# Kernel tuning notes

Hardware: AMD Instinct MI355X
Metric: run time of the kernel (lower is better)

## Reference

```python
import jax, jax.numpy as jnp
import numpy as np
from jax import lax

EPS = 1e-8
NUM_CLASSES = 10
OUT_DIM = 16
IN_CAPS = 32 * 6 * 6  # 1152
IN_DIM = 8
NUM_ITERS = 3


def squash(x, axis=-1):
    norm = jnp.sum(x * x, axis=axis, keepdims=True)
    return norm / (norm + 1.0) * x / (jnp.sqrt(norm) + EPS)


def conv2d(x, w, b, stride):
    y = lax.conv_general_dilated(x, w, window_strides=(stride, stride), padding='VALID',
                                 dimension_numbers=('NCHW', 'OIHW', 'NCHW'))
    return y + b[None, :, None, None]


def setup_inputs() -> dict:
    key = jax.random.key(0)
    ks = jax.random.split(key, 12)
    B = 256
    inp = {}
    inp['x'] = jax.random.normal(ks[0], (B, 1, 28, 28), dtype=jnp.float32)
    inp['y'] = jax.random.randint(ks[1], (B,), 0, NUM_CLASSES)
    s = 0.05
    inp['conv1_w'] = jax.random.normal(ks[2], (256, 1, 9, 9), dtype=jnp.float32) * s
    inp['conv1_b'] = jnp.zeros((256,), dtype=jnp.float32)
    inp['prim_w'] = jax.random.normal(ks[3], (32 * 8, 256, 9, 9), dtype=jnp.float32) * s
    inp['prim_b'] = jnp.zeros((32 * 8,), dtype=jnp.float32)
    # torch init is randn; scaled down mildly for numerical sanity
    inp['route_W'] = jax.random.normal(ks[4], (NUM_CLASSES, IN_CAPS, IN_DIM, OUT_DIM), dtype=jnp.float32) * 0.1
    inp['dec_w1'] = jax.random.normal(ks[5], (NUM_CLASSES * OUT_DIM, 512), dtype=jnp.float32) * s
    inp['dec_b1'] = jnp.zeros((512,), dtype=jnp.float32)
    inp['dec_w2'] = jax.random.normal(ks[6], (512, 1024), dtype=jnp.float32) * s
    inp['dec_b2'] = jnp.zeros((1024,), dtype=jnp.float32)
    inp['dec_w3'] = jax.random.normal(ks[7], (1024, 28 * 28), dtype=jnp.float32) * s
    inp['dec_b3'] = jnp.zeros((28 * 28,), dtype=jnp.float32)
    return inp


def reference(x, y, conv1_w, conv1_b, prim_w, prim_b, route_W,
              dec_w1, dec_b1, dec_w2, dec_b2, dec_w3, dec_b3):
    B = x.shape[0]
    # conv1 + relu: [B,256,20,20]
    h = jax.nn.relu(conv2d(x, conv1_w, conv1_b, stride=1))
    # primary capsules: conv stride 2 -> [B,256,6,6] -> [B,1152,8], squash
    p = conv2d(h, prim_w, prim_b, stride=2)
    u = squash(p.reshape(B, -1, IN_DIM))  # [B,1152,8]
    # routing: u_hat [B,C,N,D]
    u_hat = jnp.einsum('bnd,cnde->bcne', u, route_W)
    b_logits = jnp.zeros_like(u_hat)
    for _ in range(NUM_ITERS - 1):
        c = jax.nn.softmax(b_logits, axis=2)
        s = jnp.sum(c * u_hat, axis=2, keepdims=True)  # [B,C,1,D]
        v = squash(s)
        b_logits = b_logits + u_hat * v
    c = jax.nn.softmax(b_logits, axis=2)
    s = jnp.sum(c * u_hat, axis=2, keepdims=True)
    v = squash(s)[:, :, 0, :]  # [B,C,D]
    logits = jax.nn.softmax(jnp.sqrt(jnp.sum(v * v, axis=-1)), axis=-1)  # [B,C]
    y_onehot = jax.nn.one_hot(y, NUM_CLASSES, dtype=v.dtype)  # [B,C]
    d = (v * y_onehot[:, :, None]).reshape(B, -1)  # [B,160]
    d = jax.nn.relu(d @ dec_w1 + dec_b1)
    d = jax.nn.relu(d @ dec_w2 + dec_b2)
    recons = d @ dec_w3 + dec_b3  # [B,784]
    return logits, recons
```

## Files before the change

### kernel.cpp

```cpp
#include <hip/hip_runtime.h>
#include <hip/hip_fp16.h>
#include <math.h>

#define EPS 1e-8f
#define AS1 __attribute__((address_space(1)))
#define AS3 __attribute__((address_space(3)))

typedef _Float16 f16x8 __attribute__((ext_vector_type(8)));
typedef float f32x4 __attribute__((ext_vector_type(4)));

__global__ __launch_bounds__(256) void transpose_k(const float* __restrict__ in,
                                                   float* __restrict__ out, int R, int C) {
    __shared__ float tile[64][65];
    int tx = threadIdx.x & 63, ty = threadIdx.x >> 6;
    int c0 = blockIdx.x * 64, r0 = blockIdx.y * 64;
#pragma unroll
    for (int i = 0; i < 16; ++i) {
        int r = r0 + ty + i * 4, c = c0 + tx;
        if (r < R && c < C) tile[ty + i * 4][tx] = in[(long)r * C + c];
    }
    __syncthreads();
#pragma unroll
    for (int i = 0; i < 16; ++i) {
        int r = c0 + ty + i * 4, c = r0 + tx;
        if (r < C && c < R) out[(long)r * R + c] = tile[tx][ty + i * 4];
    }
}

__global__ __launch_bounds__(256) void wprep_k(const float* __restrict__ prim_w,
                                               __half* __restrict__ w2) {
    __shared__ float pl[128 * 81];
    int t = threadIdx.x, co = blockIdx.x, cih = blockIdx.y;
    for (int i = t; i < 10368; i += 256) pl[i] = prim_w[co * 20736 + cih * 10368 + i];
    __syncthreads();
    for (int o = t; o < 10368; o += 256) {
        int tap = o >> 7, cil = o & 127;
        w2[(long)co * 20736 + tap * 256 + cih * 128 + cil] = __float2half(pl[cil * 81 + tap]);
    }
}

__global__ __launch_bounds__(256) void conv1_k(const float* __restrict__ x,
                                               const float* __restrict__ wt1,
                                               const float* __restrict__ bias,
                                               __half* __restrict__ hh) {
    __shared__ float img[784];
    __shared__ float wl2[81 * 128];
    int t = threadIdx.x, b = blockIdx.x;
    int chalf = blockIdx.y >> 1, ph = blockIdx.y & 1;
    for (int i = t; i < 784; i += 256) img[i] = x[b * 784 + i];
    for (int i = t; i < 81 * 128; i += 256) {
        int tap = i >> 7, j = i & 127;
        wl2[i] = wt1[tap * 256 + chalf * 128 + j];
    }
    __syncthreads();
    int lane = t & 63, grp = t >> 6;
    int col = lane * 2;
    float2 cb = *(const float2*)&bias[chalf * 128 + col];
    int ow0 = ph * 10;
    for (int oh = grp * 5; oh < grp * 5 + 5; ++oh) {
        float acc0[10], acc1[10];
#pragma unroll
        for (int p = 0; p < 10; ++p) { acc0[p] = 0.f; acc1[p] = 0.f; }
#pragma unroll
        for (int kh = 0; kh < 9; ++kh) {
            float r[19];
            const float* irow = &img[(oh + kh) * 28 + ow0];
#pragma unroll
            for (int q = 0; q < 19; ++q) r[q] = irow[q];
#pragma unroll
            for (int kw = 0; kw < 9; ++kw) {
                float2 wv = *(const float2*)&wl2[(kh * 9 + kw) * 128 + col];
#pragma unroll
                for (int p = 0; p < 10; ++p) {
                    acc0[p] += r[kw + p] * wv.x;
                    acc1[p] += r[kw + p] * wv.y;
                }
            }
        }
#pragma unroll
        for (int p = 0; p < 10; ++p) {
            int pix = oh * 20 + ow0 + p;
            __half2 hv;
            hv.x = __float2half(fmaxf(acc0[p] + cb.x, 0.f));
            hv.y = __float2half(fmaxf(acc1[p] + cb.y, 0.f));
            *(__half2*)&hh[((long)b * 400 + pix) * 256 + chalf * 128 + col] = hv;
        }
    }
}

__global__ __launch_bounds__(256) void primgemm_k(const __half* __restrict__ hh,
                                                  const __half* __restrict__ w2,
                                                  float* __restrict__ Cpart) {
    __shared__ __align__(16) char lds[2][32768];
    const int t = threadIdx.x;
    const int lane = t & 63, w = t >> 6;
    const int l15 = lane & 15, kl = lane >> 4;
    const int sw = l15 & 7;

    const int bx = blockIdx.x;
    const int mt = bx >> 3, nb = (bx >> 2) & 1, ks = bx & 3;
    const int mr = w >> 1, nc = w & 1;

    long wsrc[4], asrc[4];
    int dstW[4];
#pragma unroll
    for (int q = 0; q < 4; ++q) {
        int row = q * 32 + w * 8 + (lane >> 3);
        int lc = (lane & 7) ^ (row & 7);
        dstW[q] = q * 4096 + w * 1024;
        wsrc[q] = (long)(nb * 128 + row) * 20736 + ks * 64 + lc * 8;
        int m = mt * 128 + row;
        int bi = m / 36, pos = m - bi * 36;
        int oy = pos / 6, ox = pos - oy * 6;
        asrc[q] = ((long)bi * 400 + oy * 40 + ox * 2) * 256 + ks * 64 + lc * 8;
    }

    f32x4 acc[4][4];
#pragma unroll
    for (int i = 0; i < 4; ++i)
#pragma unroll
        for (int j = 0; j < 4; ++j) acc[i][j] = (f32x4){0.f, 0.f, 0.f, 0.f};

    auto stage = [&](int bufi, int tap) {
        int kh = tap / 9, kw = tap - kh * 9;
        int woff = tap * 256;
        int aoff = (kh * 20 + kw) * 256;
#pragma unroll
        for (int q = 0; q < 4; ++q)
            __builtin_amdgcn_global_load_lds((const AS1 void*)(w2 + wsrc[q] + woff),
                                             (AS3 void*)(&lds[bufi][dstW[q]]), 16, 0, 0);
#pragma unroll
        for (int q = 0; q < 4; ++q)
            __builtin_amdgcn_global_load_lds((const AS1 void*)(hh + asrc[q] + aoff),
                                             (AS3 void*)(&lds[bufi][16384 + dstW[q]]), 16, 0, 0);
    };

    int wrowb[4], arowb[4], rdoff[2];
#pragma unroll
    for (int f = 0; f < 4; ++f) {
        wrowb[f] = (nc * 64 + f * 16 + l15) * 128;
        arowb[f] = 16384 + (mr * 64 + f * 16 + l15) * 128;
    }
#pragma unroll
    for (int kc = 0; kc < 2; ++kc) rdoff[kc] = ((kc * 4 + kl) ^ sw) << 4;

    stage(0, 0);
    __syncthreads();
    int buf = 0;
    for (int s = 0; s < 81; ++s) {
        if (s < 80) stage(buf ^ 1, s + 1);
        const char* B = lds[buf];
#pragma unroll
        for (int kc = 0; kc < 2; ++kc) {
            f16x8 wf[4], af[4];
#pragma unroll
            for (int nf = 0; nf < 4; ++nf) wf[nf] = *(const f16x8*)(B + wrowb[nf] + rdoff[kc]);
#pragma unroll
            for (int mf = 0; mf < 4; ++mf) af[mf] = *(const f16x8*)(B + arowb[mf] + rdoff[kc]);
#pragma unroll
            for (int mf = 0; mf < 4; ++mf)
#pragma unroll
                for (int nf = 0; nf < 4; ++nf)
                    acc[mf][nf] = __builtin_amdgcn_mfma_f32_16x16x32_f16(wf[nf], af[mf],
                                                                         acc[mf][nf], 0, 0, 0);
        }
        __syncthreads();
        buf ^= 1;
    }

    float* Cp = Cpart + (long)ks * 2359296;
#pragma unroll
    for (int mf = 0; mf < 4; ++mf)
#pragma unroll
        for (int nf = 0; nf < 4; ++nf) {
            int m = mt * 128 + mr * 64 + mf * 16 + l15;
            int co = nb * 128 + nc * 64 + nf * 16 + kl * 4;
            *(f32x4*)(Cp + (long)m * 256 + co) = acc[mf][nf];
        }
}

__global__ __launch_bounds__(256) void squashp_k(const float* __restrict__ Cpart,
                                                 const float* __restrict__ bias,
                                                 float* __restrict__ u) {
    __shared__ float sm[9216];
    __shared__ float bs[256];
    int t = threadIdx.x, b = blockIdx.x;
    bs[t] = bias[t];
    for (int i = t; i < 9216; i += 256) {
        float s = 0.f;
#pragma unroll
        for (int ks = 0; ks < 4; ++ks) s += Cpart[(long)ks * 2359296 + (long)b * 9216 + i];
        sm[i] = s;
    }
    __syncthreads();
    for (int cap = t; cap < 1152; cap += 256) {
        float xs[8], sn = 0.f;
#pragma unroll
        for (int d = 0; d < 8; ++d) {
            int f = cap * 8 + d;
            int co = f / 36, pos = f - co * 36;
            float vv = sm[pos * 256 + co] + bs[co];
            xs[d] = vv;
            sn += vv * vv;
        }
        float sc = sn / ((sn + 1.f) * (sqrtf(sn) + EPS));
#pragma unroll
        for (int d = 0; d < 8; ++d) u[(long)b * 9216 + cap * 8 + d] = xs[d] * sc;
    }
}

__global__ __launch_bounds__(256) void uhat_k(const float* __restrict__ u,
                                              const float* __restrict__ W,
                                              __half* __restrict__ uh) {
    __shared__ float wl[32 * 132];
    int t = threadIdx.x;
    int c = blockIdx.x / 36, ng = blockIdx.x - c * 36;
    const float* Wc = W + (long)c * 147456 + ng * 4096;
    for (int i = t; i < 4096; i += 256) {
        int row = i >> 7, k = i & 127;
        wl[row * 132 + k] = Wc[i];
    }
    __syncthreads();
    int nl = t >> 3, bl = t & 7;
    int n = ng * 32 + nl;
    const float* wr = &wl[nl * 132];
    for (int bq = 0; bq < 32; ++bq) {
        int b = bq * 8 + bl;
        const float* ub = u + (long)b * 9216 + n * 8;
        float4 ua = *(const float4*)ub, uv = *(const float4*)(ub + 4);
        float ud[8] = {ua.x, ua.y, ua.z, ua.w, uv.x, uv.y, uv.z, uv.w};
        float acc[16];
#pragma unroll
        for (int e = 0; e < 16; ++e) acc[e] = 0.f;
#pragma unroll
        for (int d = 0; d < 8; ++d) {
            const float* wd = wr + d * 16;
#pragma unroll
            for (int eq = 0; eq < 4; ++eq) {
                float4 wq = *(const float4*)(wd + eq * 4);
                acc[eq * 4 + 0] += ud[d] * wq.x;
                acc[eq * 4 + 1] += ud[d] * wq.y;
                acc[eq * 4 + 2] += ud[d] * wq.z;
                acc[eq * 4 + 3] += ud[d] * wq.w;
            }
        }
        f16x8 o0, o1;
#pragma unroll
        for (int e = 0; e < 8; ++e) {
            o0[e] = (_Float16)acc[e];
            o1[e] = (_Float16)acc[8 + e];
        }
        __half* dst = uh + ((long)(c * 256 + b)) * 18432 + n * 16;
        *(f16x8*)dst = o0;
        *(f16x8*)(dst + 8) = o1;
    }
}

__global__ __launch_bounds__(256) void route2_k(const __half* __restrict__ uh,
                                                float* __restrict__ v) {
    __shared__ float red[4][18];
    int t = threadIdx.x;
    int c = blockIdx.x >> 8, b = blockIdx.x & 255;
    int lane = t & 63, w = t >> 6;
    const float valid4 = (t < 128) ? 1.f : 0.f;
    const __half* ub = uh + ((long)(c * 256 + b)) * 18432;

    f16x8 uhh[5][2];
#pragma unroll
    for (int i = 0; i < 5; ++i) {
        int n = (i == 4) ? ((t < 128) ? 1024 + t : 0) : (t + 256 * i);
        const __half* p = ub + n * 16;
        uhh[i][0] = *(const f16x8*)p;
        uhh[i][1] = *(const f16x8*)(p + 8);
    }

    float vsum[16], sv[16];
#pragma unroll
    for (int e = 0; e < 16; ++e) vsum[e] = 0.f;

    for (int iter = 0; iter < 3; ++iter) {
        float li[5];
        float pmax = -1e30f;
#pragma unroll
        for (int i = 0; i < 5; ++i) {
            float s = 0.f;
#pragma unroll
            for (int e = 0; e < 16; ++e) s += (float)uhh[i][e >> 3][e & 7] * vsum[e];
            li[i] = s;
            float sm = (i == 4 && valid4 == 0.f) ? -1e30f : s;
            pmax = fmaxf(pmax, sm);
        }
#pragma unroll
        for (int m = 1; m < 64; m <<= 1) pmax = fmaxf(pmax, __shfl_xor(pmax, m, 64));
        if (lane == 0) red[w][17] = pmax;
        __syncthreads();
        float M = fmaxf(fmaxf(red[0][17], red[1][17]), fmaxf(red[2][17], red[3][17]));

        float pe = 0.f, se[16];
#pragma unroll
        for (int e = 0; e < 16; ++e) se[e] = 0.f;
#pragma unroll
        for (int i = 0; i < 5; ++i) {
            float E = __expf(li[i] - M);
            if (i == 4) E *= valid4;
            pe += E;
#pragma unroll
            for (int e = 0; e < 16; ++e) se[e] += E * (float)uhh[i][e >> 3][e & 7];
        }
#pragma unroll
        for (int m = 1; m < 64; m <<= 1) {
            pe += __shfl_xor(pe, m, 64);
#pragma unroll
            for (int e = 0; e < 16; ++e) se[e] += __shfl_xor(se[e], m, 64);
        }
        if (lane == 0) {
            red[w][16] = pe;
#pragma unroll
            for (int e = 0; e < 16; ++e) red[w][e] = se[e];
        }
        __syncthreads();
        float peT = red[0][16] + red[1][16] + red[2][16] + red[3][16];
        float rp = 1.f / peT;
        float nrm = 0.f;
#pragma unroll
        for (int e = 0; e < 16; ++e) {
            sv[e] = (red[0][e] + red[1][e] + red[2][e] + red[3][e]) * rp;
            nrm += sv[e] * sv[e];
        }
        float sc = nrm / ((nrm + 1.f) * (sqrtf(nrm) + EPS));
#pragma unroll
        for (int e = 0; e < 16; ++e) {
            sv[e] *= sc;
            vsum[e] += sv[e];
        }
        __syncthreads();
    }
    if (t == 0) {
#pragma unroll
        for (int e = 0; e < 16; ++e) v[(b * 10 + c) * 16 + e] = sv[e];
    }
}

__global__ __launch_bounds__(256) void logits_k(const float* __restrict__ v,
                                                float* __restrict__ out) {
    int b = threadIdx.x;
    float nr[10];
#pragma unroll
    for (int c = 0; c < 10; ++c) {
        float s2 = 0.f;
#pragma unroll
        for (int e = 0; e < 16; ++e) {
            float xv = v[(b * 10 + c) * 16 + e];
            s2 += xv * xv;
        }
        nr[c] = sqrtf(s2);
    }
    float mx = nr[0];
#pragma unroll
    for (int c = 1; c < 10; ++c) mx = fmaxf(mx, nr[c]);
    float ex[10], sm = 0.f;
#pragma unroll
    for (int c = 0; c < 10; ++c) {
        ex[c] = __expf(nr[c] - mx);
        sm += ex[c];
    }
#pragma unroll
    for (int c = 0; c < 10; ++c) out[b * 10 + c] = ex[c] / sm;
}

__global__ __launch_bounds__(256) void fc1_k(const float* __restrict__ v,
                                             const int* __restrict__ y,
                                             const float* __restrict__ w1,
                                             const float* __restrict__ b1,
                                             float* __restrict__ h1) {
    int b = blockIdx.x, t = threadIdx.x;
    __shared__ float vs[16];
    int cls = y[b];
    if (t < 16) vs[t] = v[(b * 10 + cls) * 16 + t];
    __syncthreads();
    for (int j = t; j < 512; j += 256) {
        float a = b1[j];
#pragma unroll
        for (int d = 0; d < 16; ++d) a += vs[d] * w1[(cls * 16 + d) * 512 + j];
        h1[b * 512 + j] = fmaxf(a, 0.f);
    }
}

__global__ __launch_bounds__(256) void fc_k(const float* __restrict__ A,
                                            const float* __restrict__ Wt,
                                            const float* __restrict__ bias,
                                            float* __restrict__ C,
                                            int K, int N, int relu) {
    __shared__ float al[8 * 1024];
    int t = threadIdx.x;
    int j = blockIdx.x * 256 + t;
    int r0 = blockIdx.y * 8;
    for (int idx = t; idx < 8 * K; idx += 256) {
        int r = idx / K, kk = idx - r * K;
        al[r * K + kk] = A[(r0 + r) * K + kk];
    }
    __syncthreads();
    if (j < N) {
        float bj = bias[j];
        float acc[8];
#pragma unroll
        for (int i = 0; i < 8; ++i) acc[i] = bj;
        for (int k = 0; k < K; ++k) {
            float w = Wt[(long)k * N + j];
#pragma unroll
            for (int i = 0; i < 8; ++i) acc[i] += al[i * K + k] * w;
        }
#pragma unroll
        for (int i = 0; i < 8; ++i) {
            float o = acc[i];
            if (relu) o = fmaxf(o, 0.f);
            C[(r0 + i) * N + j] = o;
        }
    }
}

extern "C" void kernel_launch(void* const* d_in, const int* in_sizes, int n_in,
                              void* d_out, int out_size, void* d_ws, size_t ws_size,
                              hipStream_t stream) {
    (void)in_sizes; (void)n_in; (void)out_size; (void)ws_size;
    const float* x       = (const float*)d_in[0];
    const int*   y       = (const int*)d_in[1];
    const float* conv1_w = (const float*)d_in[2];
    const float* conv1_b = (const float*)d_in[3];
    const float* prim_w  = (const float*)d_in[4];
    const float* prim_b  = (const float*)d_in[5];
    const float* route_W = (const float*)d_in[6];
    const float* dec_w1  = (const float*)d_in[7];
    const float* dec_b1  = (const float*)d_in[8];
    const float* dec_w2  = (const float*)d_in[9];
    const float* dec_b2  = (const float*)d_in[10];
    const float* dec_w3  = (const float*)d_in[11];
    const float* dec_b3  = (const float*)d_in[12];
    float* out = (float*)d_out;

    float* ws  = (float*)d_ws;
    float* Cp  = ws;
    float* u   = Cp + 9437184;
    float* wt1 = u + 2359296;
    float* v   = wt1 + 20736;
    float* h1  = v + 40960;
    float* h2  = h1 + 131072;
    __half* hh = (__half*)(h2 + 262144);
    __half* w2 = hh + 26214400;
    __half* uhb = hh;

    hipLaunchKernelGGL(transpose_k, dim3(2, 4), dim3(256), 0, stream, conv1_w, wt1, 256, 81);
    hipLaunchKernelGGL(wprep_k, dim3(256, 2), dim3(256), 0, stream, prim_w, w2);
    hipLaunchKernelGGL(conv1_k, dim3(256, 4), dim3(256), 0, stream, x, wt1, conv1_b, hh);
    hipLaunchKernelGGL(primgemm_k, dim3(576), dim3(256), 0, stream, hh, w2, Cp);
    hipLaunchKernelGGL(squashp_k, dim3(256), dim3(256), 0, stream, Cp, prim_b, u);
    hipLaunchKernelGGL(uhat_k, dim3(360), dim3(256), 0, stream, u, route_W, uhb);
    hipLaunchKernelGGL(route2_k, dim3(2560), dim3(256), 0, stream, uhb, v);
    hipLaunchKernelGGL(logits_k, dim3(1), dim3(256), 0, stream, v, out);
    hipLaunchKernelGGL(fc1_k, dim3(256), dim3(256), 0, stream, v, y, dec_w1, dec_b1, h1);
    hipLaunchKernelGGL(fc_k, dim3(4, 32), dim3(256), 0, stream, h1, dec_w2, dec_b2, h2, 512, 1024, 1);
    hipLaunchKernelGGL(fc_k, dim3(4, 32), dim3(256), 0, stream, h2, dec_w3, dec_b3, out + 2560, 1024, 784, 0);
}
```

Baseline: 581.3 us.

## Load primary-capsule A operand directly into registers instead of via LDS

In the primary-capsule implicit GEMM, the activation (A) tiles are now read from global memory straight into per-lane MFMA fragment registers, double-buffered across taps, rather than staged through LDS with global_load_lds. Only the weight tile stays in LDS, which halves LDS use and removes LDS reads for A. The trade-off is more register pressure, and each wave now issues its own A loads instead of sharing a staged tile, so the same data may be fetched redundantly by the wave pairs that share rows.

```diff
diff --git a/kernel.cpp b/kernel.cpp
--- a/kernel.cpp
+++ b/kernel.cpp
@@ -91,7 +91,7 @@
 __global__ __launch_bounds__(256) void primgemm_k(const __half* __restrict__ hh,
                                                   const __half* __restrict__ w2,
                                                   float* __restrict__ Cpart) {
-    __shared__ __align__(16) char lds[2][32768];
+    __shared__ __align__(16) char lds[2][16384];
     const int t = threadIdx.x;
     const int lane = t & 63, w = t >> 6;
     const int l15 = lane & 15, kl = lane >> 4;
@@ -101,7 +101,7 @@
     const int mt = bx >> 3, nb = (bx >> 2) & 1, ks = bx & 3;
     const int mr = w >> 1, nc = w & 1;
 
-    long wsrc[4], asrc[4];
+    long wsrc[4];
     int dstW[4];
 #pragma unroll
     for (int q = 0; q < 4; ++q) {
@@ -109,10 +109,15 @@
         int lc = (lane & 7) ^ (row & 7);
         dstW[q] = q * 4096 + w * 1024;
         wsrc[q] = (long)(nb * 128 + row) * 20736 + ks * 64 + lc * 8;
-        int m = mt * 128 + row;
+    }
+
+    long abase[4];
+#pragma unroll
+    for (int mf = 0; mf < 4; ++mf) {
+        int m = mt * 128 + mr * 64 + mf * 16 + l15;
         int bi = m / 36, pos = m - bi * 36;
         int oy = pos / 6, ox = pos - oy * 6;
-        asrc[q] = ((long)bi * 400 + oy * 40 + ox * 2) * 256 + ks * 64 + lc * 8;
+        abase[mf] = ((long)bi * 400 + oy * 40 + ox * 2) * 256 + ks * 64 + kl * 8;
     }
 
     f32x4 acc[4][4];
@@ -122,51 +127,62 @@
         for (int j = 0; j < 4; ++j) acc[i][j] = (f32x4){0.f, 0.f, 0.f, 0.f};
 
     auto stage = [&](int bufi, int tap) {
-        int kh = tap / 9, kw = tap - kh * 9;
         int woff = tap * 256;
-        int aoff = (kh * 20 + kw) * 256;
 #pragma unroll
         for (int q = 0; q < 4; ++q)
             __builtin_amdgcn_global_load_lds((const AS1 void*)(w2 + wsrc[q] + woff),
                                              (AS3 void*)(&lds[bufi][dstW[q]]), 16, 0, 0);
-#pragma unroll
-        for (int q = 0; q < 4; ++q)
-            __builtin_amdgcn_global_load_lds((const AS1 void*)(hh + asrc[q] + aoff),
-                                             (AS3 void*)(&lds[bufi][16384 + dstW[q]]), 16, 0, 0);
     };
-
-    int wrowb[4], arowb[4], rdoff[2];
-#pragma unroll
-    for (int f = 0; f < 4; ++f) {
-        wrowb[f] = (nc * 64 + f * 16 + l15) * 128;
-        arowb[f] = 16384 + (mr * 64 + f * 16 + l15) * 128;
-    }
+    auto loadA = [&](f16x8 (&dst)[4][2], int tap) {
+        int kh = tap / 9, kw = tap - kh * 9;
+        int aoff = (kh * 20 + kw) * 256;
+#pragma unroll
+        for (int mf = 0; mf < 4; ++mf)
+#pragma unroll
+            for (int kc = 0; kc < 2; ++kc)
+                dst[mf][kc] = *(const f16x8*)(hh + abase[mf] + aoff + kc * 32);
+    };
+
+    int wrowb[4], rdoff[2];
+#pragma unroll
+    for (int f = 0; f < 4; ++f) wrowb[f] = (nc * 64 + f * 16 + l15) * 128;
 #pragma unroll
     for (int kc = 0; kc < 2; ++kc) rdoff[kc] = ((kc * 4 + kl) ^ sw) << 4;
 
+    auto compute = [&](const char* B, f16x8 (&ar)[4][2]) {
+#pragma unroll
+        for (int kc = 0; kc < 2; ++kc) {
+            f16x8 wf[4];
+#pragma unroll
+            for (int nf = 0; nf < 4; ++nf) wf[nf] = *(const f16x8*)(B + wrowb[nf] + rdoff[kc]);
+#pragma unroll
+            for (int mf = 0; mf < 4; ++mf)
+#pragma unroll
+                for (int nf = 0; nf < 4; ++nf)
+                    acc[mf][nf] = __builtin_amdgcn_mfma_f32_16x16x32_f16(wf[nf], ar[mf][kc],
+                                                                         acc[mf][nf], 0, 0, 0);
+        }
+    };
+
+    f16x8 aA[4][2], aB[4][2];
+    loadA(aA, 0);
     stage(0, 0);
     __syncthreads();
     int buf = 0;
-    for (int s = 0; s < 81; ++s) {
-        if (s < 80) stage(buf ^ 1, s + 1);
-        const char* B = lds[buf];
-#pragma unroll
-        for (int kc = 0; kc < 2; ++kc) {
-            f16x8 wf[4], af[4];
-#pragma unroll
-            for (int nf = 0; nf < 4; ++nf) wf[nf] = *(const f16x8*)(B + wrowb[nf] + rdoff[kc]);
-#pragma unroll
-            for (int mf = 0; mf < 4; ++mf) af[mf] = *(const f16x8*)(B + arowb[mf] + rdoff[kc]);
-#pragma unroll
-            for (int mf = 0; mf < 4; ++mf)
-#pragma unroll
-                for (int nf = 0; nf < 4; ++nf)
-                    acc[mf][nf] = __builtin_amdgcn_mfma_f32_16x16x32_f16(wf[nf], af[mf],
-                                                                         acc[mf][nf], 0, 0, 0);
-        }
+    for (int ss = 0; ss < 40; ++ss) {
+        int s = ss * 2;
+        stage(buf ^ 1, s + 1);
+        loadA(aB, s + 1);
+        compute(lds[buf], aA);
         __syncthreads();
         buf ^= 1;
-    }
+        stage(buf ^ 1, s + 2);
+        loadA(aA, s + 2);
+        compute(lds[buf], aB);
+        __syncthreads();
+        buf ^= 1;
+    }
+    compute(lds[buf], aA);
 
     float* Cp = Cpart + (long)ks * 2359296;
 #pragma unroll
```

Result: slower. 767.0 us (+31.9%).

## Double split-K in primary-capsule GEMM and simplify conv1 inner loop

Applied to the files above, without the earlier changes.

The primary-capsule GEMM now splits K eight ways instead of four, launching 1152 blocks with half-size LDS tiles (32 channels per tap) and a new XOR swizzle. The aim is more parallelism and occupancy, since smaller LDS use lets more blocks share a CU. In exchange, the partial-sum buffer doubles, so the squash kernel reads and reduces eight partials, and the workspace layout is rearranged to fit it. Conv1 drops the register-cached input row and the kh unroll, reading each image value from LDS per tap, which may lower register pressure but adds LDS reads.

```diff
diff --git a/kernel.cpp b/kernel.cpp
--- a/kernel.cpp
+++ b/kernel.cpp
@@ -61,19 +61,15 @@
         float acc0[10], acc1[10];
 #pragma unroll
         for (int p = 0; p < 10; ++p) { acc0[p] = 0.f; acc1[p] = 0.f; }
-#pragma unroll
         for (int kh = 0; kh < 9; ++kh) {
-            float r[19];
-            const float* irow = &img[(oh + kh) * 28 + ow0];
-#pragma unroll
-            for (int q = 0; q < 19; ++q) r[q] = irow[q];
-#pragma unroll
             for (int kw = 0; kw < 9; ++kw) {
-                float2 wv = *(const float2*)&wl2[(kh * 9 + kw) * 128 + col];
+                float2 w2v = *(const float2*)&wl2[(kh * 9 + kw) * 128 + col];
+                const float* irow = &img[(oh + kh) * 28 + ow0 + kw];
 #pragma unroll
                 for (int p = 0; p < 10; ++p) {
-                    acc0[p] += r[kw + p] * wv.x;
-                    acc1[p] += r[kw + p] * wv.y;
+                    float iv = irow[p];
+                    acc0[p] += iv * w2v.x;
+                    acc1[p] += iv * w2v.y;
                 }
             }
         }
@@ -91,28 +87,28 @@
 __global__ __launch_bounds__(256) void primgemm_k(const __half* __restrict__ hh,
                                                   const __half* __restrict__ w2,
                                                   float* __restrict__ Cpart) {
-    __shared__ __align__(16) char lds[2][32768];
+    __shared__ __align__(16) char lds[2][16384];
     const int t = threadIdx.x;
     const int lane = t & 63, w = t >> 6;
     const int l15 = lane & 15, kl = lane >> 4;
-    const int sw = l15 & 7;
 
     const int bx = blockIdx.x;
-    const int mt = bx >> 3, nb = (bx >> 2) & 1, ks = bx & 3;
+    const int mt = bx >> 4, nb = (bx >> 3) & 1, ks = bx & 7;
     const int mr = w >> 1, nc = w & 1;
 
-    long wsrc[4], asrc[4];
-    int dstW[4];
-#pragma unroll
-    for (int q = 0; q < 4; ++q) {
-        int row = q * 32 + w * 8 + (lane >> 3);
-        int lc = (lane & 7) ^ (row & 7);
-        dstW[q] = q * 4096 + w * 1024;
-        wsrc[q] = (long)(nb * 128 + row) * 20736 + ks * 64 + lc * 8;
+    long wsrc[2], asrc[2];
+    int dstO[2];
+#pragma unroll
+    for (int q = 0; q < 2; ++q) {
+        int slot = q * 256 + t;
+        int row = slot >> 2, pc = slot & 3;
+        int lc = pc ^ ((row >> 1) & 3);
+        dstO[q] = q * 4096 + w * 1024;
+        wsrc[q] = (long)(nb * 128 + row) * 20736 + ks * 32 + lc * 8;
         int m = mt * 128 + row;
         int bi = m / 36, pos = m - bi * 36;
         int oy = pos / 6, ox = pos - oy * 6;
-        asrc[q] = ((long)bi * 400 + oy * 40 + ox * 2) * 256 + ks * 64 + lc * 8;
+        asrc[q] = ((long)bi * 400 + oy * 40 + ox * 2) * 256 + ks * 32 + lc * 8;
     }
 
     f32x4 acc[4][4];
@@ -126,23 +122,23 @@
         int woff = tap * 256;
         int aoff = (kh * 20 + kw) * 256;
 #pragma unroll
-        for (int q = 0; q < 4; ++q)
+        for (int q = 0; q < 2; ++q)
             __builtin_amdgcn_global_load_lds((const AS1 void*)(w2 + wsrc[q] + woff),
-                                             (AS3 void*)(&lds[bufi][dstW[q]]), 16, 0, 0);
-#pragma unroll
-        for (int q = 0; q < 4; ++q)
+                                             (AS3 void*)(&lds[bufi][dstO[q]]), 16, 0, 0);
+#pragma unroll
+        for (int q = 0; q < 2; ++q)
             __builtin_amdgcn_global_load_lds((const AS1 void*)(hh + asrc[q] + aoff),
-                                             (AS3 void*)(&lds[bufi][16384 + dstW[q]]), 16, 0, 0);
+                                             (AS3 void*)(&lds[bufi][8192 + dstO[q]]), 16, 0, 0);
     };
 
-    int wrowb[4], arowb[4], rdoff[2];
+    int wro[4], aro[4];
 #pragma unroll
     for (int f = 0; f < 4; ++f) {
-        wrowb[f] = (nc * 64 + f * 16 + l15) * 128;
-        arowb[f] = 16384 + (mr * 64 + f * 16 + l15) * 128;
-    }
-#pragma unroll
-    for (int kc = 0; kc < 2; ++kc) rdoff[kc] = ((kc * 4 + kl) ^ sw) << 4;
+        int wr_ = nc * 64 + f * 16 + l15;
+        int ar_ = mr * 64 + f * 16 + l15;
+        wro[f] = wr_ * 64 + ((kl ^ ((wr_ >> 1) & 3)) << 4);
+        aro[f] = 8192 + ar_ * 64 + ((kl ^ ((ar_ >> 1) & 3)) << 4);
+    }
 
     stage(0, 0);
     __syncthreads();
@@ -150,20 +146,17 @@
     for (int s = 0; s < 81; ++s) {
         if (s < 80) stage(buf ^ 1, s + 1);
         const char* B = lds[buf];
-#pragma unroll
-        for (int kc = 0; kc < 2; ++kc) {
-            f16x8 wf[4], af[4];
-#pragma unroll
-            for (int nf = 0; nf < 4; ++nf) wf[nf] = *(const f16x8*)(B + wrowb[nf] + rdoff[kc]);
-#pragma unroll
-            for (int mf = 0; mf < 4; ++mf) af[mf] = *(const f16x8*)(B + arowb[mf] + rdoff[kc]);
-#pragma unroll
-            for (int mf = 0; mf < 4; ++mf)
-#pragma unroll
-                for (int nf = 0; nf < 4; ++nf)
-                    acc[mf][nf] = __builtin_amdgcn_mfma_f32_16x16x32_f16(wf[nf], af[mf],
-                                                                         acc[mf][nf], 0, 0, 0);
-        }
+        f16x8 wf[4], af[4];
+#pragma unroll
+        for (int nf = 0; nf < 4; ++nf) wf[nf] = *(const f16x8*)(B + wro[nf]);
+#pragma unroll
+        for (int mf = 0; mf < 4; ++mf) af[mf] = *(const f16x8*)(B + aro[mf]);
+#pragma unroll
+        for (int mf = 0; mf < 4; ++mf)
+#pragma unroll
+            for (int nf = 0; nf < 4; ++nf)
+                acc[mf][nf] = __builtin_amdgcn_mfma_f32_16x16x32_f16(wf[nf], af[mf],
+                                                                     acc[mf][nf], 0, 0, 0);
         __syncthreads();
         buf ^= 1;
     }
@@ -189,7 +182,7 @@
     for (int i = t; i < 9216; i += 256) {
         float s = 0.f;
 #pragma unroll
-        for (int ks = 0; ks < 4; ++ks) s += Cpart[(long)ks * 2359296 + (long)b * 9216 + i];
+        for (int ks = 0; ks < 8; ++ks) s += Cpart[(long)ks * 2359296 + (long)b * 9216 + i];
         sm[i] = s;
     }
     __syncthreads();
@@ -440,19 +433,19 @@
 
     float* ws  = (float*)d_ws;
     float* Cp  = ws;
-    float* u   = Cp + 9437184;
+    __half* hh = (__half*)(ws + 18874368);
+    __half* w2 = hh + 26214400;
+    float* u   = ws + 18874368 + 13107200 + 2654208;
     float* wt1 = u + 2359296;
     float* v   = wt1 + 20736;
     float* h1  = v + 40960;
     float* h2  = h1 + 131072;
-    __half* hh = (__half*)(h2 + 262144);
-    __half* w2 = hh + 26214400;
-    __half* uhb = hh;
+    __half* uhb = (__half*)ws;
 
     hipLaunchKernelGGL(transpose_k, dim3(2, 4), dim3(256), 0, stream, conv1_w, wt1, 256, 81);
     hipLaunchKernelGGL(wprep_k, dim3(256, 2), dim3(256), 0, stream, prim_w, w2);
     hipLaunchKernelGGL(conv1_k, dim3(256, 4), dim3(256), 0, stream, x, wt1, conv1_b, hh);
-    hipLaunchKernelGGL(primgemm_k, dim3(576), dim3(256), 0, stream, hh, w2, Cp);
+    hipLaunchKernelGGL(primgemm_k, dim3(1152), dim3(256), 0, stream, hh, w2, Cp);
     hipLaunchKernelGGL(squashp_k, dim3(256), dim3(256), 0, stream, Cp, prim_b, u);
     hipLaunchKernelGGL(uhat_k, dim3(360), dim3(256), 0, stream, u, route_W, uhb);
     hipLaunchKernelGGL(route2_k, dim3(2560), dim3(256), 0, stream, uhb, v);
```

Measured after the change: 626.0 us. 7.7% more time.
